# Kernel optimization log

Measured on AMD Instinct MI355X. Metric: run time of the kernel, lower is better.

## Reference

```python
import jax, jax.numpy as jnp
import numpy as np

IN_DIM, OUT_DIM = 256, 10
N_EXPERTS, N_MEM, STEPS, N_SUB, MAX_K = 12, 32, 6, 5, 5
EXPERT_DIMS = [2048, 2560, 3072, 3584, 4096, 2304, 2816, 3328, 3840, 4608, 3072, 4096]
MAX_E = 4608
N_ITEMS = 4096
SCALE = IN_DIM ** -0.5

def _gelu(x):
    return jax.nn.gelu(x, approximate=False)

_ACTS = [jax.nn.silu, _gelu, lambda x: x * jnp.tanh(jax.nn.softplus(x)), jax.nn.relu,
         jax.nn.selu, jnp.tanh, jax.nn.softplus, jax.nn.elu]
EXPERT_ACTS = [_ACTS[i % 8] for i in range(N_EXPERTS)]

def _ln(x, s, b, eps=1e-5):
    mu = jnp.mean(x, -1, keepdims=True)
    var = jnp.mean((x - mu) ** 2, -1, keepdims=True)
    return (x - mu) * jax.lax.rsqrt(var + eps) * s + b

def _cell(x, ln_s, ln_b, w1, b1, w2, b2):
    h = _gelu(_ln(x, ln_s, ln_b) @ w1.T + b1)
    return x + h @ w2.T + b2

def _ctx_attn(cur, bank, qw, kw, vw):
    q = cur @ qw.T
    k = bank @ kw.T
    v = bank @ vw.T
    attn = jax.nn.softmax(jnp.einsum('nd,ntd->nt', q, k) * SCALE, axis=-1)
    return jnp.einsum('nt,ntd->nd', attn, v)

def _renorm_sparse_topk(probs, active_k):
    tv, ti = jax.lax.top_k(probs, MAX_K)
    mask = (jnp.arange(MAX_K)[None, :] < active_k[:, None]).astype(probs.dtype)
    vals = tv * mask
    rows = jnp.arange(probs.shape[0])[:, None]
    sparse = jnp.zeros_like(probs).at[rows, ti].set(vals)
    return sparse / jnp.maximum(jnp.sum(sparse, -1, keepdims=True), 1e-6)

def _fwd(x, W, b,
         shared_up_w, shared_down_w, shared_ln_s, shared_ln_b, shared_scale,
         mem_keys, mem_vals, mem_q_w, mem_out_w, mem_wg_w, mem_wg_b, mem_wv_w, mem_wv_b,
         depth_q_w, depth_k_w, depth_v_w, depth_out_w,
         rc_ln_s, rc_ln_b, rc_w1, rc_b1, rc_w2, rc_b2,
         ssm_in_w, ssm_out_w, ssm_decay,
         sub_w, sub_b, gate_w, gate_b,
         budget_w, budget_b,
         exp_up, exp_down, exp_ln_s, exp_ln_b,
         halt_w, halt_b,
         aux_up_w, aux_down_w, aux_ln_s, aux_ln_b, aux_gate_w, aux_gate_b,
         rf_ln_s, rf_ln_b, rf_w1, rf_b1, rf_w2, rf_b2, reflect_out_w,
         coll_q_w, coll_k_w, coll_v_w, coll_out_w,
         revisit_w, revisit_b,
         vc_ln_s, vc_ln_b, vc_w1, vc_b1, vc_w2, vc_b2,
         ver_q_w, ver_k_w, ver_v_w, ver_out_w, ver_gate_w, ver_gate_b, correction_out_w,
         mix):
    n = x.shape[0]
    base = x @ W.T + b
    shared = _ln(jax.nn.silu(x @ shared_up_w.T) @ shared_down_w.T, shared_ln_s, shared_ln_b)
    aux = _ln(_gelu(x @ aux_up_w.T) @ aux_down_w.T, aux_ln_s, aux_ln_b)

    mem_vals_b = jnp.broadcast_to(mem_vals[None], (n, N_MEM, IN_DIM))
    current = x
    mem_logits = jnp.zeros_like(base)
    depth_logits = jnp.zeros_like(base)
    cum_halt = jnp.zeros((n, 1), x.dtype)
    bank = []
    for s in range(STEPS):
        q = current @ mem_q_w.T
        attn = jax.nn.softmax((q @ mem_keys.T) * SCALE, axis=-1)
        mem_read = jnp.einsum('ns,nsd->nd', attn, mem_vals_b)
        wg = jax.nn.sigmoid(jnp.concatenate([current, mem_read], -1) @ mem_wg_w.T + mem_wg_b)
        wv = current @ mem_wv_w.T + mem_wv_b
        mem_vals_b = mem_vals_b * (1.0 - wg[..., None]) + wg[..., None] * wv[:, None, :]
        if bank:
            depth_ctx = _ctx_attn(current, jnp.stack(bank, 1), depth_q_w, depth_k_w, depth_v_w)
        else:
            depth_ctx = jnp.zeros_like(current)
        current = _cell(current + mem_read + depth_ctx,
                        rc_ln_s[s], rc_ln_b[s], rc_w1[s], rc_b1[s], rc_w2[s], rc_b2[s])
        h = jnp.tanh(current @ ssm_in_w.T) * jax.nn.sigmoid(ssm_decay)
        current = current + h @ ssm_out_w.T
        bank.append(current)
        halt = jax.nn.sigmoid((current @ halt_w[s])[:, None] + halt_b[s])
        w_step = (1.0 - cum_halt) * halt
        mem_logits = mem_logits + w_step * (mem_read @ mem_out_w.T)
        depth_logits = depth_logits + w_step * (depth_ctx @ depth_out_w.T)
        cum_halt = jnp.minimum(cum_halt + halt, 1.0)

    sub_logits = jnp.einsum('nd,sed->nse', current, sub_w) + sub_b
    sub_probs = jax.nn.softmax(sub_logits, axis=-1)
    gate = jax.nn.softmax(current @ gate_w.T + gate_b, axis=-1)
    probs = jnp.einsum('ns,nse->ne', gate, sub_probs)
    active_k = jnp.argmax(current @ budget_w.T + budget_b, axis=-1) + 1
    sparse = _renorm_sparse_topk(probs, active_k)

    expert_out = jnp.zeros_like(base)
    for i in range(N_EXPERTS):
        h = EXPERT_ACTS[i](current @ exp_up[i].T)
        o = _ln(h @ exp_down[i].T, exp_ln_s[i], exp_ln_b[i])
        expert_out = expert_out + sparse[:, i:i + 1] * o

    r = current
    for i in range(3):
        r = _cell(r, rf_ln_s[i], rf_ln_b[i], rf_w1[i], rf_b1[i], rf_w2[i], rf_b2[i])
    reflect_logits = r @ reflect_out_w.T

    stack = jnp.stack(bank, 1)
    coll_ctx = _ctx_attn(current, stack, coll_q_w, coll_k_w, coll_v_w)
    coll_logits = coll_ctx @ coll_out_w.T
    revisit = jax.nn.sigmoid(jnp.concatenate([x, current, coll_ctx], -1) @ revisit_w.T + revisit_b)

    v = current
    for i in range(2):
        v = _cell(v, vc_ln_s[i], vc_ln_b[i], vc_w1[i], vc_b1[i], vc_w2[i], vc_b2[i])
    ver_ctx = _ctx_attn(v, stack, ver_q_w, ver_k_w, ver_v_w)
    vg = jax.nn.softmax(jnp.concatenate([v, ver_ctx], -1) @ ver_gate_w.T + ver_gate_b, axis=-1)
    ver_logits = ver_ctx @ ver_out_w.T
    corr_logits = v @ correction_out_w.T

    ag = jax.nn.softmax(x @ aux_gate_w.T + aux_gate_b, axis=-1)
    alpha, beta, gamma, delta, eps_, zeta = [jnp.tanh(mix[i]) for i in range(6)]
    logits = (base
              + shared_scale * (ag[:, :1] * shared + ag[:, 1:] * aux)
              + alpha * expert_out
              + beta * mem_logits + zeta * depth_logits
              + gamma * reflect_logits
              + delta * revisit * coll_logits
              + eps_ * (vg[:, :1] * ver_logits + vg[:, 1:] * corr_logits))
    return logits


def setup_inputs() -> dict:
    key = jax.random.key(0)
    ks = iter(jax.random.split(key, 128))
    def nrm(shape, std=0.02):
        return jax.random.normal(next(ks), shape, jnp.float32) * std
    d, o = IN_DIM, OUT_DIM
    inp = dict(
        x=jax.random.normal(next(ks), (N_ITEMS, d), jnp.float32),
        W=nrm((o, d), 0.05), b=jnp.zeros((o,), jnp.float32),
        shared_up_w=nrm((3072, d)), shared_down_w=nrm((o, 3072)),
        shared_ln_s=jnp.ones((o,)), shared_ln_b=jnp.zeros((o,)),
        shared_scale=jnp.float32(1.0),
        mem_keys=nrm((N_MEM, d)), mem_vals=nrm((N_MEM, d)),
        mem_q_w=nrm((d, d), 0.01), mem_out_w=nrm((o, d), 0.01),
        mem_wg_w=nrm((N_MEM, 2 * d), 0.01), mem_wg_b=jnp.zeros((N_MEM,)),
        mem_wv_w=nrm((d, d), 0.01), mem_wv_b=jnp.zeros((d,)),
        depth_q_w=nrm((d, d), 0.01), depth_k_w=nrm((d, d), 0.01),
        depth_v_w=nrm((d, d), 0.01), depth_out_w=nrm((o, d), 0.01),
        rc_ln_s=jnp.ones((STEPS, d)), rc_ln_b=jnp.zeros((STEPS, d)),
        rc_w1=nrm((STEPS, 896, d)), rc_b1=jnp.zeros((STEPS, 896)),
        rc_w2=nrm((STEPS, d, 896)), rc_b2=jnp.zeros((STEPS, d)),
        ssm_in_w=nrm((48, d)), ssm_out_w=nrm((d, 48)), ssm_decay=jnp.zeros((48,)),
        sub_w=nrm((N_SUB, N_EXPERTS, d)), sub_b=jnp.zeros((N_SUB, N_EXPERTS)),
        gate_w=nrm((N_SUB, d)), gate_b=jnp.zeros((N_SUB,)),
        budget_w=nrm((MAX_K, d), 0.01), budget_b=jnp.zeros((MAX_K,)),
        halt_w=nrm((STEPS, d), 0.01), halt_b=jnp.full((STEPS,), -2.0, jnp.float32),
        aux_up_w=nrm((4096, d)), aux_down_w=nrm((o, 4096)),
        aux_ln_s=jnp.ones((o,)), aux_ln_b=jnp.zeros((o,)),
        aux_gate_w=nrm((2, d), 0.01), aux_gate_b=jnp.zeros((2,)),
        rf_ln_s=jnp.ones((3, d)), rf_ln_b=jnp.zeros((3, d)),
        rf_w1=nrm((3, 1280, d)), rf_b1=jnp.zeros((3, 1280)),
        rf_w2=nrm((3, d, 1280)), rf_b2=jnp.zeros((3, d)),
        reflect_out_w=nrm((o, d), 0.01),
        coll_q_w=nrm((d, d), 0.01), coll_k_w=nrm((d, d), 0.01),
        coll_v_w=nrm((d, d), 0.01), coll_out_w=nrm((o, d), 0.01),
        revisit_w=nrm((1, 3 * d), 0.01), revisit_b=jnp.zeros((1,)),
        vc_ln_s=jnp.ones((2, d)), vc_ln_b=jnp.zeros((2, d)),
        vc_w1=nrm((2, 1536, d)), vc_b1=jnp.zeros((2, 1536)),
        vc_w2=nrm((2, d, 1536)), vc_b2=jnp.zeros((2, d)),
        ver_q_w=nrm((d, d), 0.01), ver_k_w=nrm((d, d), 0.01),
        ver_v_w=nrm((d, d), 0.01), ver_out_w=nrm((o, d), 0.01),
        ver_gate_w=nrm((2, 2 * d), 0.01), ver_gate_b=jnp.zeros((2,)),
        correction_out_w=nrm((o, d), 0.01),
        mix=jnp.full((6,), 0.5, jnp.float32),
    )
    up = jax.random.normal(next(ks), (N_EXPERTS, MAX_E, d), jnp.float32) * 0.02
    down = jax.random.normal(next(ks), (N_EXPERTS, o, MAX_E), jnp.float32) * 0.01
    col = jnp.arange(MAX_E)
    dims = jnp.array(EXPERT_DIMS)
    mask = (col[None, :] < dims[:, None]).astype(jnp.float32)
    inp['exp_up'] = up * mask[:, :, None]
    inp['exp_down'] = down * mask[:, None, :]
    inp['exp_ln_s'] = jnp.ones((N_EXPERTS, o))
    inp['exp_ln_b'] = jnp.zeros((N_EXPERTS, o))
    return inp


def reference(x, W, b,
              shared_up_w, shared_down_w, shared_ln_s, shared_ln_b, shared_scale,
              mem_keys, mem_vals, mem_q_w, mem_out_w, mem_wg_w, mem_wg_b, mem_wv_w, mem_wv_b,
              depth_q_w, depth_k_w, depth_v_w, depth_out_w,
              rc_ln_s, rc_ln_b, rc_w1, rc_b1, rc_w2, rc_b2,
              ssm_in_w, ssm_out_w, ssm_decay,
              sub_w, sub_b, gate_w, gate_b,
              budget_w, budget_b,
              exp_up, exp_down, exp_ln_s, exp_ln_b,
              halt_w, halt_b,
              aux_up_w, aux_down_w, aux_ln_s, aux_ln_b, aux_gate_w, aux_gate_b,
              rf_ln_s, rf_ln_b, rf_w1, rf_b1, rf_w2, rf_b2, reflect_out_w,
              coll_q_w, coll_k_w, coll_v_w, coll_out_w,
              revisit_w, revisit_b,
              vc_ln_s, vc_ln_b, vc_w1, vc_b1, vc_w2, vc_b2,
              ver_q_w, ver_k_w, ver_v_w, ver_out_w, ver_gate_w, ver_gate_b, correction_out_w,
              mix):
    return _fwd(x, W, b,
                shared_up_w, shared_down_w, shared_ln_s, shared_ln_b, shared_scale,
                mem_keys, mem_vals, mem_q_w, mem_out_w, mem_wg_w, mem_wg_b, mem_wv_w, mem_wv_b,
                depth_q_w, depth_k_w, depth_v_w, depth_out_w,
                rc_ln_s, rc_ln_b, rc_w1, rc_b1, rc_w2, rc_b2,
                ssm_in_w, ssm_out_w, ssm_decay,
                sub_w, sub_b, gate_w, gate_b,
                budget_w, budget_b,
                exp_up, exp_down, exp_ln_s, exp_ln_b,
                halt_w, halt_b,
                aux_up_w, aux_down_w, aux_ln_s, aux_ln_b, aux_gate_w, aux_gate_b,
                rf_ln_s, rf_ln_b, rf_w1, rf_b1, rf_w2, rf_b2, reflect_out_w,
                coll_q_w, coll_k_w, coll_v_w, coll_out_w,
                revisit_w, revisit_b,
                vc_ln_s, vc_ln_b, vc_w1, vc_b1, vc_w2, vc_b2,
                ver_q_w, ver_k_w, ver_v_w, ver_out_w, ver_gate_w, ver_gate_b, correction_out_w,
                mix)
```

## Files before the change

### kernel.cpp

```cpp
#include <hip/hip_runtime.h>


constexpr int NI      = 4096;
constexpr int DIM     = 256;
constexpr int ODIM    = 10;
constexpr int NMEM_   = 32;
constexpr int NSTEPS_ = 6;
constexpr int NEXPERT_= 12;
constexpr int MAXE    = 4608;
constexpr int TOTCOL  = 46592;
#define SCL 0.0625f

__constant__ int GCNT[14]   = {8,10,12,14,16,9,11,13,15,18,12,16,12,16};
__constant__ int GSTART[14] = {0,8,18,30,44,60,69,80,93,108,126,138,154,166};
__constant__ int CCNT[14]   = {32,40,48,56,64,36,44,52,60,72,48,64,48,64};
__constant__ int ZCOL[14]   = {0,2048,4608,7680,11264,15360,17664,20480,
                               23808,27648,32256,35328,39424,42496};

typedef __attribute__((ext_vector_type(8))) short short8v;
typedef __attribute__((ext_vector_type(4))) float float4v;
typedef __attribute__((ext_vector_type(4))) unsigned short ushort4v;


__device__ __forceinline__ float wred_sum(float v){
// ... 113 lines not shown
    #pragma unroll
    for (int h = 0; h < 2; ++h){
      int kk = lkq + h*4;
      float4 va = *(const float4*)&A[(size_t)(bm+lrow)*K + k0 + kk];
      float4 vw = *(const float4*)&W[(size_t)(bn+lrow)*K + k0 + kk];
      As[kk+0][lrow]=va.x; As[kk+1][lrow]=va.y; As[kk+2][lrow]=va.z; As[kk+3][lrow]=va.w;
      Ws[kk+0][lrow]=vw.x; Ws[kk+1][lrow]=vw.y; Ws[kk+2][lrow]=vw.z; Ws[kk+3][lrow]=vw.w;
    }
    __syncthreads();
    #pragma unroll
    for (int kk = 0; kk < 32; ++kk){
      float4 a4 = *(const float4*)&As[kk][ty*4];
      float4 b4 = *(const float4*)&Ws[kk][tx*4];
      float av[4] = {a4.x,a4.y,a4.z,a4.w};
      float bv[4] = {b4.x,b4.y,b4.z,b4.w};
      #pragma unroll
      for (int i=0;i<4;i++)
        #pragma unroll
        for (int j=0;j<4;j++) acc[i][j] = fmaf(av[i], bv[j], acc[i][j]);
    }
    __syncthreads();
  }
  #pragma unroll
  for (int i=0;i<4;i++){
    int r = bm + ty*4 + i;
    #pragma unroll
    for (int j=0;j<4;j++){
      int c = bn + tx*4 + j;
      float v = acc[i][j];
      if constexpr (EPI==0){ C[(size_t)r*N + c] = v; }
      else if constexpr (EPI==1){ C[(size_t)r*N + c] = v + bias[c]; }
      else if constexpr (EPI==3){ C[(size_t)r*N + c] = v + bias[c] + R[(size_t)r*N + c]; }
      else if constexpr (EPI==6){
        if (c < 256) C[(size_t)r*256 + c] = v + bias[c];
        else C2[(size_t)r*256 + (c-256)] = v;
      }
    }
  }
}

__global__ __launch_bounds__(256)
void gemm_rc1_k(const float* __restrict__ A, const float* __restrict__ W,
                const float* __restrict__ bias, float* __restrict__ C,
                int N, int K)
{
  __shared__ float As[32][132];
  __shared__ float Ws[32][68];
  const int bm = blockIdx.y*128, bn = blockIdx.x*64;
  const int tid = threadIdx.x;
  const int tx = tid & 15, ty = tid >> 4;
  const int arow = tid >> 1, ak = (tid & 1)*16;
  const int brow = tid >> 2, bk = (tid & 3)*8;
  float acc[8][4] = {};
  for (int k0 = 0; k0 < K; k0 += 32){
    float4 a0 = *(const float4*)&A[(size_t)(bm+arow)*K + k0 + ak];
    float4 a1 = *(const float4*)&A[(size_t)(bm+arow)*K + k0 + ak + 4];
    float4 a2 = *(const float4*)&A[(size_t)(bm+arow)*K + k0 + ak + 8];
    float4 a3 = *(const float4*)&A[(size_t)(bm+arow)*K + k0 + ak + 12];
    float4 b0 = *(const float4*)&W[(size_t)(bn+brow)*K + k0 + bk];
    float4 b1 = *(const float4*)&W[(size_t)(bn+brow)*K + k0 + bk + 4];
    As[ak+ 0][arow]=a0.x; As[ak+ 1][arow]=a0.y; As[ak+ 2][arow]=a0.z; As[ak+ 3][arow]=a0.w;
    As[ak+ 4][arow]=a1.x; As[ak+ 5][arow]=a1.y; As[ak+ 6][arow]=a1.z; As[ak+ 7][arow]=a1.w;
    As[ak+ 8][arow]=a2.x; As[ak+ 9][arow]=a2.y; As[ak+10][arow]=a2.z; As[ak+11][arow]=a2.w;
    As[ak+12][arow]=a3.x; As[ak+13][arow]=a3.y; As[ak+14][arow]=a3.z; As[ak+15][arow]=a3.w;
    Ws[bk+0][brow]=b0.x; Ws[bk+1][brow]=b0.y; Ws[bk+2][brow]=b0.z; Ws[bk+3][brow]=b0.w;
    Ws[bk+4][brow]=b1.x; Ws[bk+5][brow]=b1.y; Ws[bk+6][brow]=b1.z; Ws[bk+7][brow]=b1.w;
    __syncthreads();
    #pragma unroll
    for (int kk = 0; kk < 32; ++kk){
      float a8[8];
      *(float4*)&a8[0] = *(const float4*)&As[kk][ty*8];
      *(float4*)&a8[4] = *(const float4*)&As[kk][ty*8+4];
      float4 b4 = *(const float4*)&Ws[kk][tx*4];
      float bv[4] = {b4.x,b4.y,b4.z,b4.w};
      #pragma unroll
      for (int i=0;i<8;i++)
        #pragma unroll
        for (int j=0;j<4;j++) acc[i][j] = fmaf(a8[i], bv[j], acc[i][j]);
    }
    __syncthreads();
  }
  #pragma unroll
  for (int i=0;i<8;i++){
    int r = bm + ty*8 + i;
    #pragma unroll
    for (int j=0;j<4;j++){
      int c = bn + tx*4 + j;
      C[(size_t)r*N + c] = geluf(acc[i][j] + bias[c]);
    }
  }
}

template<int EPI>
__global__ __launch_bounds__(256)
void bgemm_k(const short* __restrict__ A, const short* __restrict__ B,
             const float* __restrict__ bias, const float* __restrict__ R,
             float* __restrict__ Cf, unsigned short* __restrict__ Cb,
             int N, int K)
{
  __shared__ short As[128][40];
  __shared__ short Bsm[64][40];
  const int bm = blockIdx.y*128, bn = blockIdx.x*64;
  const int tid = threadIdx.x;
  const int wave = tid >> 6, lane = tid & 63;
  const int l15 = lane & 15, lg = lane >> 4;
  const int ar = tid >> 1, ah = tid & 1;
  float4v acc[2][4] = {};
  for (int k0 = 0; k0 < K; k0 += 32){
    __syncthreads();
    { const short* src = A + (size_t)(bm+ar)*K + k0 + ah*16;
      short8v v0 = *(const short8v*)src;
      short8v v1 = *(const short8v*)(src+8);
      *(short8v*)&As[ar][ah*16]   = v0;
      *(short8v*)&As[ar][ah*16+8] = v1; }
    if (tid < 128){
      const short* src = B + (size_t)(bn+ar)*K + k0 + ah*16;
      short8v v0 = *(const short8v*)src;
      short8v v1 = *(const short8v*)(src+8);
      *(short8v*)&Bsm[ar][ah*16]   = v0;
      *(short8v*)&Bsm[ar][ah*16+8] = v1; }
    __syncthreads();
    short8v bfr[4];
    #pragma unroll
    for (int nt = 0; nt < 4; nt++)
      bfr[nt] = *(const short8v*)&Bsm[nt*16 + l15][lg*8];
    #pragma unroll
    for (int mt = 0; mt < 2; mt++){
      short8v a = *(const short8v*)&As[wave*32 + mt*16 + l15][lg*8];
      #pragma unroll
      for (int nt = 0; nt < 4; nt++)
        acc[mt][nt] = __builtin_amdgcn_mfma_f32_16x16x32_bf16(a, bfr[nt], acc[mt][nt], 0, 0, 0);
    }
  }
  #pragma unroll
  for (int mt = 0; mt < 2; mt++)
    #pragma unroll
    for (int nt = 0; nt < 4; nt++)
      #pragma unroll
      for (int reg = 0; reg < 4; reg++){
        int row = bm + wave*32 + mt*16 + lg*4 + reg;
        int col = bn + nt*16 + l15;
        float v = acc[mt][nt][reg];
        if constexpr (EPI==0){
          v = geluf(v + bias[col]);
          Cb[(size_t)row*N + col] = f2b(v);
        } else {
          v = v + bias[col] + R[(size_t)row*N + col];
          Cf[(size_t)row*N + col] = v;
        }
      }
}

__global__ __launch_bounds__(512)
void moe7_k(const unsigned short* __restrict__ curb, const unsigned short* __restrict__ xb,
            const short* __restrict__ upb,
            const float* __restrict__ exp_down, const float* __restrict__ shared_down,
            const float* __restrict__ aux_down,
            const int* __restrict__ idxl, const int* __restrict__ cnt,
            unsigned short* __restrict__ part)
{
  __shared__ short Bs[16384];
  __shared__ float Ds[64][12];
  int gy = blockIdx.y, z = 0;
  while (gy >= GCNT[z]){ gy -= GCNT[z]; z++; }
  const int n = (z < 12) ? cnt[z] : NI;
  const int bm = blockIdx.x*128;
  if (bm >= n) return;
  const int g = GSTART[z] + gy;
  const int localcol = gy*256;
  int act, dstride; const float* down;
  if (z < 12){ act = z & 7; down = exp_down + (size_t)z*ODIM*MAXE; dstride = MAXE; }
  else if (z == 12){ act = 0; down = shared_down; dstride = 3072; }
  else { act = 1; down = aux_down; dstride = 4096; }
  const unsigned short* X = (z < 12) ? curb : xb;
  const int tid = threadIdx.x, wave = tid >> 6, lane = tid & 63;
  const int l15 = lane & 15, lg = lane >> 4;

  int slotA = bm + wave*16 + l15;
  int itemA;
  if (z < 12) itemA = idxl[(size_t)z*NI + ((slotA < n) ? slotA : (n-1))];
  else        itemA = slotA;

  short8v afrag[8];
  { const unsigned short* xr = X + (size_t)itemA*DIM;
    #pragma unroll
    for (int ks = 0; ks < 8; ks++)
      afrag[ks] = *(const short8v*)&xr[ks*32 + lg*8];
  }
  float racc[4][10];
  #pragma unroll
  for (int r = 0; r < 4; r++)
    #pragma unroll
    for (int o = 0; o < 10; o++) racc[r][o] = 0.f;

  const int gchunk0 = (ZCOL[z] + localcol) >> 6;
  const int dso = tid >> 6, dse = tid & 63;

  short8v p0, p1, p2, p3;
  float e0, e1;
  auto ldchunk = [&](int ch){
    const short* chunk = upb + ((size_t)(gchunk0 + ch))*16384;
    p0 = *(const short8v*)&chunk[(size_t)(tid       )*8];
    p1 = *(const short8v*)&chunk[(size_t)(tid +  512)*8];
    p2 = *(const short8v*)&chunk[(size_t)(tid + 1024)*8];
    p3 = *(const short8v*)&chunk[(size_t)(tid + 1536)*8];
    int cb = localcol + ch*64;
    e0 = down[(size_t)dso*dstride + cb + dse];
    e1 = (tid < 128) ? down[(size_t)(dso+8)*dstride + cb + dse] : 0.f;
  };
  auto stu = [&](int u, short8v v){
    int c = u & 63, kq = u >> 6;
    int byteoff = ((c << 9) + (kq << 4)) ^ ((c & 7) << 4);
    *(short8v*)((char*)Bs + byteoff) = v;
  };

  ldchunk(0);
  for (int ch = 0; ch < 4; ++ch){
    stu(tid, p0); stu(tid + 512, p1); stu(tid + 1024, p2); stu(tid + 1536, p3);
    Ds[dse][dso] = e0;
    if (tid < 128) Ds[dse][dso + 8] = e1;
    __syncthreads();
    if (ch < 3) ldchunk(ch + 1);
    float4v acc[4] = {};
    #pragma unroll
    for (int ks = 0; ks < 8; ks++)
      #pragma unroll
      for (int nt = 0; nt < 4; nt++){
        int c = nt*16 + l15, kq = ks*4 + lg;
        int byteoff = ((c << 9) + (kq << 4)) ^ ((c & 7) << 4);
        short8v b = *(const short8v*)((const char*)Bs + byteoff);
        acc[nt] = __builtin_amdgcn_mfma_f32_16x16x32_bf16(afrag[ks], b, acc[nt], 0, 0, 0);
      }
    float hv[4][4];
    switch(act){
      case 0:
        #pragma unroll
        for (int nt=0;nt<4;nt++)
          #pragma unroll
          for (int r=0;r<4;r++){ float xx=acc[nt][r]; hv[nt][r]=xx*sigm(xx); }
        break;
      case 1:
        #pragma unroll
        for (int nt=0;nt<4;nt++)
          #pragma unroll
          for (int r=0;r<4;r++){ hv[nt][r]=geluf(acc[nt][r]); }
        break;
      case 2:
        #pragma unroll
        for (int nt=0;nt<4;nt++)
          #pragma unroll
          for (int r=0;r<4;r++){ float xx=acc[nt][r]; hv[nt][r]=xx*tanh_f(softplusf(xx)); }
        break;
      case 3:
        #pragma unroll
        for (int nt=0;nt<4;nt++)
          #pragma unroll
          for (int r=0;r<4;r++){ hv[nt][r]=fmaxf(acc[nt][r],0.f); }
        break;
      case 4:
        #pragma unroll
        for (int nt=0;nt<4;nt++)
          #pragma unroll
          for (int r=0;r<4;r++){
            const float l=1.0507009873554805f, al=1.6732632423543772f;
            float xx=acc[nt][r];
            hv[nt][r] = xx>0.f ? l*xx : l*al*(__expf(xx)-1.f);
          }
        break;
      case 5:
        #pragma unroll
        for (int nt=0;nt<4;nt++)
          #pragma unroll
          for (int r=0;r<4;r++){ hv[nt][r]=tanh_f(acc[nt][r]); }
        break;
      case 6:
        #pragma unroll
        for (int nt=0;nt<4;nt++)
          #pragma unroll
          for (int r=0;r<4;r++){ hv[nt][r]=softplusf(acc[nt][r]); }
        break;
      default:
        #pragma unroll
        for (int nt=0;nt<4;nt++)
          #pragma unroll
          for (int r=0;r<4;r++){ float xx=acc[nt][r]; hv[nt][r]= xx>0.f ? xx : __expf(xx)-1.f; }
        break;
    }
    #pragma unroll
    for (int nt = 0; nt < 4; nt++){
      const float* dp = &Ds[nt*16 + l15][0];
      float4 dv0 = *(const float4*)dp;
      float4 dv1 = *(const float4*)(dp + 4);
      float  d8 = dp[8], d9 = dp[9];
      float dv[10] = {dv0.x,dv0.y,dv0.z,dv0.w,dv1.x,dv1.y,dv1.z,dv1.w,d8,d9};
      #pragma unroll
      for (int o = 0; o < 10; o++)
        #pragma unroll
        for (int r = 0; r < 4; r++)
          racc[r][o] = fmaf(hv[nt][r], dv[o], racc[r][o]);
    }
    __syncthreads();
  }
  #pragma unroll
  for (int r = 0; r < 4; r++)
    #pragma unroll
    for (int o = 0; o < 10; o++){
      float v = racc[r][o];
      v += __shfl_xor(v, 1, 64); v += __shfl_xor(v, 2, 64);
      v += __shfl_xor(v, 4, 64); v += __shfl_xor(v, 8, 64);
      racc[r][o] = v;
    }
  if (l15 == 0){
    #pragma unroll
    for (int r = 0; r < 4; r++){
      int slotW = bm + wave*16 + lg*4 + r;
      int itemW;
      if (z < 12) itemW = idxl[(size_t)z*NI + ((slotW < n) ? slotW : (n-1))];
      else        itemW = slotW;
      #pragma unroll
      for (int o = 0; o < 10; o++)
        part[((size_t)g*NI + itemW)*ODIM + o] = f2b(racc[r][o]);
    }
  }
}

__global__ __launch_bounds__(256)
void red_k(const unsigned short* __restrict__ part, float* __restrict__ expert_pre,
           float* __restrict__ shared_pre, float* __restrict__ aux_pre)
{
  int idx = blockIdx.x*256 + threadIdx.x;
  if (idx >= 14*NI*ODIM) return;
  int z = idx / (NI*ODIM), rem = idx - z*NI*ODIM;
  float s = 0.f;
  int g0 = GSTART[z], gn = GCNT[z];
  for (int g2 = 0; g2 < gn; g2++)
    s += b2f(part[(size_t)(g0 + g2)*NI*ODIM + rem]);
  if (z < 12) expert_pre[(size_t)z*NI*ODIM + rem] = s;
  else if (z == 12) shared_pre[rem] = s;
  else aux_pre[rem] = s;
}

__global__ void atb_k(const float* __restrict__ A, const float* __restrict__ B,
                      float* __restrict__ C, int M, int I, int J)
{
  int idx = blockIdx.x*256 + threadIdx.x;
  if (idx >= I*J) return;
  int i = idx / J, j = idx - i*J;
  float s = 0.f;
  for (int m = 0; m < M; m++) s = fmaf(A[(size_t)m*I+i], B[(size_t)m*J+j], s);
  C[idx] = s;
}
__global__ void ab_k(const float* __restrict__ A, const float* __restrict__ B,
                     float* __restrict__ C, int M, int K, int N)
{
  int idx = blockIdx.x*256 + threadIdx.x;
  if (idx >= M*N) return;
  int i = idx / N, j = idx - i*N;
  float s = 0.f;
  for (int k = 0; k < K; k++) s = fmaf(A[(size_t)i*K+k], B[(size_t)k*N+j], s);
  C[idx] = s;
}

__global__ __launch_bounds__(256)
void ln3_k(const float* __restrict__ a, const float* __restrict__ b,
           const float* __restrict__ c, const float* __restrict__ lns,
           const float* __restrict__ lnb, float* __restrict__ xout,
           float* __restrict__ lnout, unsigned short* __restrict__ lnout_b)
{
  int item = blockIdx.x*4 + (threadIdx.x >> 6);
  int lane = threadIdx.x & 63;
  float4 v = ((const float4*)(a + (size_t)item*DIM))[lane];
  if (b){ float4 t = ((const float4*)(b + (size_t)item*DIM))[lane]; v.x+=t.x; v.y+=t.y; v.z+=t.z; v.w+=t.w; }
  if (c){ float4 t = ((const float4*)(c + (size_t)item*DIM))[lane]; v.x+=t.x; v.y+=t.y; v.z+=t.z; v.w+=t.w; }
  if (xout) ((float4*)(xout + (size_t)item*DIM))[lane] = v;
  float mu = wred_sum(v.x+v.y+v.z+v.w) * (1.f/DIM);
  float dx=v.x-mu, dy=v.y-mu, dz=v.z-mu, dw=v.w-mu;
  float var = wred_sum(dx*dx+dy*dy+dz*dz+dw*dw) * (1.f/DIM);
  float rs = 1.f/sqrtf(var + 1e-5f);
  float4 s4 = ((const float4*)lns)[lane];
  float4 b4 = ((const float4*)lnb)[lane];
  float4 o4 = make_float4(dx*rs*s4.x + b4.x, dy*rs*s4.y + b4.y,
                          dz*rs*s4.z + b4.z, dw*rs*s4.w + b4.w);
  if (lnout) ((float4*)(lnout + (size_t)item*DIM))[lane] = o4;
  if (lnout_b){
    ushort4v t; t[0]=f2b(o4.x); t[1]=f2b(o4.y); t[2]=f2b(o4.z); t[3]=f2b(o4.w);
    *(ushort4v*)(lnout_b + (size_t)item*DIM + lane*4) = t;
  }
}

__global__ __launch_bounds__(256)
void memrw_k(const float* __restrict__ cur, const float* __restrict__ MK,
             const float* __restrict__ mem_vals, const float* __restrict__ wv_hist,
             const float* __restrict__ mem_wg_w, const float* __restrict__ mem_wg_b,
             float* __restrict__ a_state, float* __restrict__ c_state,
             float* __restrict__ mem_read, int step)
{
  __shared__ float smem[4][DIM];
  int wi = threadIdx.x >> 6;
  int item = blockIdx.x*4 + wi;
  int lane = threadIdx.x & 63;
  float v = -1e30f;
  if (lane < NMEM_)
    v = dot256f(cur + (size_t)item*DIM, MK + (size_t)lane*DIM, 0.f) * SCL;
  float m = wred_max(v);
  float e = (lane < NMEM_) ? __expf(v - m) : 0.f;
  float inv = 1.f / wred_sum(e);
  float attn = e * inv;
  float aval = 0.f;
  if (lane < NMEM_) aval = (step == 0) ? 1.f : a_state[(size_t)item*NMEM_ + lane];
  float wslot = attn * aval;
  float beta[NSTEPS_];
  #pragma unroll
  for (int t = 0; t < NSTEPS_; t++){
    beta[t] = 0.f;
    if (t < step){
      float cc = (lane < NMEM_) ? c_state[((size_t)item*NMEM_ + lane)*NSTEPS_ + t] : 0.f;
      beta[t] = wred_sum(attn * cc);
    }
  }
  float ax=0.f, ay=0.f, az=0.f, aw=0.f;
  #pragma unroll
  for (int s2 = 0; s2 < NMEM_; s2++){
    float ws = __shfl(wslot, s2, 64);
    float4 mv = ((const float4*)(mem_vals + (size_t)s2*DIM))[lane];
    ax = fmaf(ws, mv.x, ax); ay = fmaf(ws, mv.y, ay);
    az = fmaf(ws, mv.z, az); aw = fmaf(ws, mv.w, aw);
  }
  #pragma unroll
  for (int t = 0; t < NSTEPS_; t++){
    if (t < step){
      float4 h4 = ((const float4*)(wv_hist + ((size_t)t*NI + item)*DIM))[lane];
      ax = fmaf(beta[t], h4.x, ax); ay = fmaf(beta[t], h4.y, ay);
      az = fmaf(beta[t], h4.z, az); aw = fmaf(beta[t], h4.w, aw);
    }
  }
  float4 mr = make_float4(ax,ay,az,aw);
  ((float4*)(mem_read + (size_t)item*DIM))[lane] = mr;
  ((float4*)&smem[wi][0])[lane] = mr;
  __syncthreads();
  if (lane < NMEM_){
    const float* wr = mem_wg_w + (size_t)lane*2*DIM;
    float s = dot256f(cur + (size_t)item*DIM, wr, 0.f);
    s = dot256f(&smem[wi][0], wr + DIM, s);
    s += mem_wg_b[lane];
    float gte = sigm(s);
    int idx = item*NMEM_ + lane;
    float om = 1.f - gte;
    float a = (step == 0) ? 1.f : a_state[idx];
    a_state[idx] = a * om;
    float* c = c_state + (size_t)idx*NSTEPS_;
    #pragma unroll
    for (int t = 0; t < NSTEPS_; t++) if (t < step) c[t] *= om;
    c[step] = gte;
  }
// ... 346 lines not shown
  const float* budget_w      = (const float*)d_in[33];
  const float* budget_b      = (const float*)d_in[34];
  const float* halt_w        = (const float*)d_in[35];
  const float* halt_b        = (const float*)d_in[36];
  const float* aux_up_w      = (const float*)d_in[37];
  const float* aux_down_w    = (const float*)d_in[38];
  const float* aux_ln_s      = (const float*)d_in[39];
  const float* aux_ln_b      = (const float*)d_in[40];
  const float* aux_gate_w    = (const float*)d_in[41];
  const float* aux_gate_b    = (const float*)d_in[42];
  const float* rf_ln_s       = (const float*)d_in[43];
  const float* rf_ln_b       = (const float*)d_in[44];
  const float* rf_w1         = (const float*)d_in[45];
  const float* rf_b1         = (const float*)d_in[46];
  const float* rf_w2         = (const float*)d_in[47];
  const float* rf_b2         = (const float*)d_in[48];
  const float* reflect_out_w = (const float*)d_in[49];
  const float* coll_q_w      = (const float*)d_in[50];
  const float* coll_k_w      = (const float*)d_in[51];
  const float* coll_v_w      = (const float*)d_in[52];
  const float* coll_out_w    = (const float*)d_in[53];
  const float* revisit_w     = (const float*)d_in[54];
  const float* revisit_b     = (const float*)d_in[55];
  const float* vc_ln_s       = (const float*)d_in[56];
  const float* vc_ln_b       = (const float*)d_in[57];
  const float* vc_w1         = (const float*)d_in[58];
  const float* vc_b1         = (const float*)d_in[59];
  const float* vc_w2         = (const float*)d_in[60];
  const float* vc_b2         = (const float*)d_in[61];
  const float* ver_q_w       = (const float*)d_in[62];
  const float* ver_k_w       = (const float*)d_in[63];
  const float* ver_v_w       = (const float*)d_in[64];
  const float* ver_out_w     = (const float*)d_in[65];
  const float* ver_gate_w    = (const float*)d_in[66];
  const float* ver_gate_b    = (const float*)d_in[67];
  const float* correction_out_w = (const float*)d_in[68];
  const float* mix           = (const float*)d_in[69];
  const float* exp_up        = (const float*)d_in[70];
  const float* exp_down      = (const float*)d_in[71];
  const float* exp_ln_s      = (const float*)d_in[72];
  const float* exp_ln_b      = (const float*)d_in[73];
  float* out = (float*)d_out;

  float* w = (float*)d_ws;
  size_t off = 0;
  auto WS = [&](size_t nf){ float* p = w + off; off += nf; return p; };
  float* bank      = WS((size_t)NSTEPS_*NI*DIM);
  float* rbuf      = WS((size_t)NI*DIM);
  float* vbuf      = WS((size_t)NI*DIM);
  float* coll_ctx  = WS((size_t)NI*DIM);
  float* ver_ctx   = WS((size_t)NI*DIM);
  float* q2        = WS((size_t)NI*DIM);
  float* wsumb     = WS((size_t)NI*DIM);
  float* sparse    = WS((size_t)NI*NEXPERT_);
  float* base10    = WS((size_t)NI*ODIM);
  float* reflect10 = WS((size_t)NI*ODIM);
  float* coll10    = WS((size_t)NI*ODIM);
  float* ver10     = WS((size_t)NI*ODIM);
  float* corr10    = WS((size_t)NI*ODIM);
  float* PcT       = WS((size_t)DIM*DIM);
  float* PvT       = WS((size_t)DIM*DIM);
  float* MK        = WS((size_t)NMEM_*DIM);
  float* Wvq       = WS((size_t)512*DIM);
  float* expert_pre= WS((size_t)NEXPERT_*NI*ODIM);
  float* shared_pre= WS((size_t)NI*ODIM);
  float* aux_pre   = WS((size_t)NI*ODIM);
  unsigned short* cur_b = (unsigned short*)WS((size_t)NI*DIM/2);
  unsigned short* x_b   = (unsigned short*)WS((size_t)NI*DIM/2);
  int* idxl        = (int*)WS((size_t)NEXPERT_*NI);
  float* S72       = WS((size_t)NI*72);
  int* cnt         = (int*)WS(16);
  float* zbase     = w + off;
  float* mem_logits   = WS((size_t)NI*ODIM);
  float* depth_logits = WS((size_t)NI*ODIM);
  float* cum_halt     = WS((size_t)NI);
  size_t zbytes = (size_t)((w + off) - zbase) * sizeof(float);
  hipMemsetAsync((void*)zbase, 0, zbytes, stream);

  float* U = w + off;
  float* wv_hist   = U;
  float* hbig      = U + (size_t)NSTEPS_*NI*DIM;
  float* cur_in    = hbig + (size_t)NI*896;
  float* t_ln      = cur_in + (size_t)NI*DIM;
  float* mem_read  = t_ln + (size_t)NI*DIM;
  float* depth_ctx = mem_read + (size_t)NI*DIM;
  float* a_state   = depth_ctx + (size_t)NI*DIM;
  float* c_state   = a_state + (size_t)NI*NMEM_;
  unsigned short* upb    = (unsigned short*)U;
  unsigned short* hb     = (unsigned short*)U;
  float* ovl = U + 5963776;
  unsigned short* t_ln_b = (unsigned short*)ovl;          ovl += 524288;
  unsigned short* rfw1b  = (unsigned short*)ovl;          ovl += 491520;
  unsigned short* rfw2b  = (unsigned short*)ovl;          ovl += 491520;
  unsigned short* vcw1b  = (unsigned short*)ovl;          ovl += 393216;
  unsigned short* vcw2b  = (unsigned short*)ovl;          ovl += 393216;
  unsigned short* part   = (unsigned short*)ovl;

  hipMemcpyAsync(Wvq, mem_wv_w, (size_t)DIM*DIM*sizeof(float),
                 hipMemcpyDeviceToDevice, stream);
  atb_k<<<(DIM*DIM+255)/256, 256, 0, stream>>>(depth_k_w, depth_q_w, Wvq + (size_t)DIM*DIM, DIM, DIM, DIM);
  atb_k<<<(DIM*DIM+255)/256, 256, 0, stream>>>(coll_k_w,  coll_q_w,  PcT, DIM, DIM, DIM);
  atb_k<<<(DIM*DIM+255)/256, 256, 0, stream>>>(ver_k_w,   ver_q_w,   PvT, DIM, DIM, DIM);
  ab_k <<<(NMEM_*DIM+255)/256, 256, 0, stream>>>(mem_keys, mem_q_w, MK, NMEM_, DIM, DIM);

  const float* cur = x;
  for (int s = 0; s < NSTEPS_; s++){
    memrw_k<<<NI/4, 256, 0, stream>>>(cur, MK, mem_vals, wv_hist,
                                      mem_wg_w, mem_wg_b, a_state, c_state,
                                      mem_read, s);
    if (s == 0){
      gemm_k<1><<<dim3(4, NI/64), 256, 0, stream>>>(
          cur, Wvq, mem_wv_b, nullptr, wv_hist, nullptr, DIM, DIM);
    } else if (s == NSTEPS_-1){
      gemm_k<0><<<dim3(4, NI/64), 256, 0, stream>>>(
          cur, Wvq + (size_t)DIM*DIM, nullptr, nullptr, q2, nullptr, DIM, DIM);
    } else {
      gemm_k<6><<<dim3(8, NI/64), 256, 0, stream>>>(
          cur, Wvq, mem_wv_b, nullptr, wv_hist + (size_t)s*NI*DIM, q2, 512, DIM);
    }
    if (s > 0){
      bankattn_k<<<NI/4, 256, 0, stream>>>(q2, bank, wsumb, s);
      gemm_k<0><<<dim3(4, NI/64), 256, 0, stream>>>(
          wsumb, depth_v_w, nullptr, nullptr, depth_ctx, nullptr, DIM, DIM);
    }
    ln3_k<<<NI/4, 256, 0, stream>>>(cur, mem_read, (s > 0 ? depth_ctx : nullptr),
                                    rc_ln_s + (size_t)s*DIM, rc_ln_b + (size_t)s*DIM,
                                    cur_in, t_ln, nullptr);
    gemm_rc1_k<<<dim3(14, NI/128), 256, 0, stream>>>(
        t_ln, rc_w1 + (size_t)s*896*DIM, rc_b1 + (size_t)s*896, hbig, 896, DIM);
    gemm_k<3><<<dim3(4, NI/64), 256, 0, stream>>>(
        hbig, rc_w2 + (size_t)s*DIM*896, rc_b2 + (size_t)s*DIM, cur_in,
        cur_in, nullptr, DIM, 896);
    float* newcur = bank + (size_t)s*NI*DIM;
    ssmhalt_k<<<NI/4, 256, 0, stream>>>(cur_in, mem_read, depth_ctx,
                                        ssm_in_w, ssm_out_w, ssm_decay,
                                        halt_w, halt_b, mem_out_w, depth_out_w,
                                        newcur, mem_logits, depth_logits, cum_halt, s);
    cur = newcur;
  }

  thin70_k<<<(NI*70 + 255)/256, 256, 0, stream>>>(
      cur, sub_w, sub_b, gate_w, gate_b, budget_w, budget_b, S72);
  topk_k<<<(NI + 255)/256, 256, 0, stream>>>(S72, sparse);
  buildlist_k<<<NEXPERT_, 256, 0, stream>>>(sparse, idxl, cnt);

  launch_cvt(cur, cur_b, (size_t)NI*DIM, stream);
  launch_cvt(x,   x_b,   (size_t)NI*DIM, stream);
  cvtup_k<<<TOTCOL/64, 512, 0, stream>>>(exp_up, shared_up_w, aux_up_w, (short*)upb);
  launch_cvt(rf_w1, rfw1b, (size_t)3*1280*DIM, stream);
  launch_cvt(rf_w2, rfw2b, (size_t)3*DIM*1280, stream);
  launch_cvt(vc_w1, vcw1b, (size_t)2*1536*DIM, stream);
  launch_cvt(vc_w2, vcw2b, (size_t)2*DIM*1536, stream);

  moe7_k<<<dim3(NI/128, 182), 512, 0, stream>>>(
      cur_b, x_b, (const short*)upb, exp_down, shared_down_w, aux_down_w,
      idxl, cnt, part);
  red_k<<<(14*NI*ODIM + 255)/256, 256, 0, stream>>>(part, expert_pre, shared_pre, aux_pre);

  const float* rsrc = cur;
  for (int i = 0; i < 3; i++){
    ln3_k<<<NI/4, 256, 0, stream>>>(rsrc, nullptr, nullptr,
                                    rf_ln_s + (size_t)i*DIM, rf_ln_b + (size_t)i*DIM,
                                    nullptr, nullptr, t_ln_b);
    bgemm_k<0><<<dim3(1280/64, NI/128), 256, 0, stream>>>(
        (const short*)t_ln_b, (const short*)(rfw1b + (size_t)i*1280*DIM),
        rf_b1 + (size_t)i*1280, nullptr, nullptr, hb, 1280, DIM);
    bgemm_k<1><<<dim3(DIM/64, NI/128), 256, 0, stream>>>(
        (const short*)hb, (const short*)(rfw2b + (size_t)i*DIM*1280),
        rf_b2 + (size_t)i*DIM, rsrc, rbuf, nullptr, DIM, 1280);
    rsrc = rbuf;
  }

  const float* vsrc = cur;
  for (int i = 0; i < 2; i++){
    ln3_k<<<NI/4, 256, 0, stream>>>(vsrc, nullptr, nullptr,
                                    vc_ln_s + (size_t)i*DIM, vc_ln_b + (size_t)i*DIM,
                                    nullptr, nullptr, t_ln_b);
    bgemm_k<0><<<dim3(1536/64, NI/128), 256, 0, stream>>>(
        (const short*)t_ln_b, (const short*)(vcw1b + (size_t)i*1536*DIM),
        vc_b1 + (size_t)i*1536, nullptr, nullptr, hb, 1536, DIM);
    bgemm_k<1><<<dim3(DIM/64, NI/128), 256, 0, stream>>>(
        (const short*)hb, (const short*)(vcw2b + (size_t)i*DIM*1536),
        vc_b2 + (size_t)i*DIM, vsrc, vbuf, nullptr, DIM, 1536);
    vsrc = vbuf;
  }

  gemm_k<0><<<dim3(4, NI/64), 256, 0, stream>>>(
      cur, PcT, nullptr, nullptr, q2, nullptr, DIM, DIM);
  bankattn_k<<<NI/4, 256, 0, stream>>>(q2, bank, wsumb, NSTEPS_);
  gemm_k<0><<<dim3(4, NI/64), 256, 0, stream>>>(
      wsumb, coll_v_w, nullptr, nullptr, coll_ctx, nullptr, DIM, DIM);

  gemm_k<0><<<dim3(4, NI/64), 256, 0, stream>>>(
      vbuf, PvT, nullptr, nullptr, q2, nullptr, DIM, DIM);
  bankattn_k<<<NI/4, 256, 0, stream>>>(q2, bank, wsumb, NSTEPS_);
  gemm_k<0><<<dim3(4, NI/64), 256, 0, stream>>>(
      wsumb, ver_v_w, nullptr, nullptr, ver_ctx, nullptr, DIM, DIM);

  heads_k<<<(NI*50 + 255)/256, 256, 0, stream>>>(
      rbuf, coll_ctx, ver_ctx, vbuf, x,
      reflect_out_w, coll_out_w, ver_out_w, correction_out_w, Wm, bvec,
      reflect10, coll10, ver10, corr10, base10);

  final_k<<<(NI+255)/256, 256, 0, stream>>>(
      x, cur, vbuf, coll_ctx, ver_ctx,
      base10, shared_pre, aux_pre, expert_pre, sparse,
      mem_logits, depth_logits, reflect10, coll10, ver10, corr10,
      shared_ln_s, shared_ln_b, aux_ln_s, aux_ln_b, exp_ln_s, exp_ln_b,
      aux_gate_w, aux_gate_b, ver_gate_w, ver_gate_b, revisit_w, revisit_b,
      shared_scale, mix, out);
}
```

Baseline: 2.769 ms.

## Read MoE up-weight fragments directly from global memory instead of LDS staging

The MoE expert kernel drops its shared-memory staging of the bf16 up-projection chunk and the down-projection slice. Each wave now loads its MFMA B fragments and down weights straight from global memory, and the chunk loop is unrolled with no block barriers. This removes the LDS writes and reads and the two __syncthreads per chunk, and frees LDS so more blocks can be resident. In exchange, all 8 waves of a block fetch the same 32KB chunk redundantly through cache, and the explicit prefetch-ahead double buffering is lost.

```diff
diff --git a/kernel.cpp b/kernel.cpp
--- a/kernel.cpp
+++ b/kernel.cpp
@@ -289,15 +289,13 @@
 }
 
 __global__ __launch_bounds__(512)
-void moe7_k(const unsigned short* __restrict__ curb, const unsigned short* __restrict__ xb,
+void moe8_k(const unsigned short* __restrict__ curb, const unsigned short* __restrict__ xb,
             const short* __restrict__ upb,
             const float* __restrict__ exp_down, const float* __restrict__ shared_down,
             const float* __restrict__ aux_down,
             const int* __restrict__ idxl, const int* __restrict__ cnt,
             unsigned short* __restrict__ part)
 {
-  __shared__ short Bs[16384];
-  __shared__ float Ds[64][12];
   int gy = blockIdx.y, z = 0;
   while (gy >= GCNT[z]){ gy -= GCNT[z]; z++; }
   const int n = (z < 12) ? cnt[z] : NI;
@@ -331,41 +329,18 @@
     for (int o = 0; o < 10; o++) racc[r][o] = 0.f;
 
   const int gchunk0 = (ZCOL[z] + localcol) >> 6;
-  const int dso = tid >> 6, dse = tid & 63;
-
-  short8v p0, p1, p2, p3;
-  float e0, e1;
-  auto ldchunk = [&](int ch){
-    const short* chunk = upb + ((size_t)(gchunk0 + ch))*16384;
-    p0 = *(const short8v*)&chunk[(size_t)(tid       )*8];
-    p1 = *(const short8v*)&chunk[(size_t)(tid +  512)*8];
-    p2 = *(const short8v*)&chunk[(size_t)(tid + 1024)*8];
-    p3 = *(const short8v*)&chunk[(size_t)(tid + 1536)*8];
-    int cb = localcol + ch*64;
-    e0 = down[(size_t)dso*dstride + cb + dse];
-    e1 = (tid < 128) ? down[(size_t)(dso+8)*dstride + cb + dse] : 0.f;
-  };
-  auto stu = [&](int u, short8v v){
-    int c = u & 63, kq = u >> 6;
-    int byteoff = ((c << 9) + (kq << 4)) ^ ((c & 7) << 4);
-    *(short8v*)((char*)Bs + byteoff) = v;
-  };
-
-  ldchunk(0);
+
+  #pragma unroll
   for (int ch = 0; ch < 4; ++ch){
-    stu(tid, p0); stu(tid + 512, p1); stu(tid + 1024, p2); stu(tid + 1536, p3);
-    Ds[dse][dso] = e0;
-    if (tid < 128) Ds[dse][dso + 8] = e1;
-    __syncthreads();
-    if (ch < 3) ldchunk(ch + 1);
+    const short* chunk = upb + (size_t)(gchunk0 + ch)*16384;
+    const int cb = localcol + ch*64;
     float4v acc[4] = {};
     #pragma unroll
     for (int ks = 0; ks < 8; ks++)
       #pragma unroll
       for (int nt = 0; nt < 4; nt++){
-        int c = nt*16 + l15, kq = ks*4 + lg;
-        int byteoff = ((c << 9) + (kq << 4)) ^ ((c & 7) << 4);
-        short8v b = *(const short8v*)((const char*)Bs + byteoff);
+        int u = (ks*4 + lg)*64 + nt*16 + l15;
+        short8v b = *(const short8v*)&chunk[(size_t)u*8];
         acc[nt] = __builtin_amdgcn_mfma_f32_16x16x32_bf16(afrag[ks], b, acc[nt], 0, 0, 0);
       }
     float hv[4][4];
@@ -425,18 +400,16 @@
     }
     #pragma unroll
     for (int nt = 0; nt < 4; nt++){
-      const float* dp = &Ds[nt*16 + l15][0];
-      float4 dv0 = *(const float4*)dp;
-      float4 dv1 = *(const float4*)(dp + 4);
-      float  d8 = dp[8], d9 = dp[9];
-      float dv[10] = {dv0.x,dv0.y,dv0.z,dv0.w,dv1.x,dv1.y,dv1.z,dv1.w,d8,d9};
+      int col = cb + nt*16 + l15;
+      float dv[10];
+      #pragma unroll
+      for (int o = 0; o < 10; o++) dv[o] = down[(size_t)o*dstride + col];
       #pragma unroll
       for (int o = 0; o < 10; o++)
         #pragma unroll
         for (int r = 0; r < 4; r++)
           racc[r][o] = fmaf(hv[nt][r], dv[o], racc[r][o]);
     }
-    __syncthreads();
   }
   #pragma unroll
   for (int r = 0; r < 4; r++)
@@ -1089,7 +1062,7 @@
   launch_cvt(vc_w1, vcw1b, (size_t)2*1536*DIM, stream);
   launch_cvt(vc_w2, vcw2b, (size_t)2*DIM*1536, stream);
 
-  moe7_k<<<dim3(NI/128, 182), 512, 0, stream>>>(
+  moe8_k<<<dim3(NI/128, 182), 512, 0, stream>>>(
       cur_b, x_b, (const short*)upb, exp_down, shared_down_w, aux_down_w,
       idxl, cnt, part);
   red_k<<<(14*NI*ODIM + 255)/256, 256, 0, stream>>>(part, expert_pre, shared_pre, aux_pre);
```

After: 3.069 ms. 10.8% more time.
